# Performance work log

Measured on AMD Instinct MI355X. Metric: run time of the kernel, lower is better.

The kernel has to match this reference:

```python
import jax, jax.numpy as jnp
import numpy as np

N_NODES = 50000
N_EDGES = 600000


def gcn_conv(x, src, dst, W, b, num_nodes):
    # x: [N, Cin] -> [N, Cout]; symmetric-normalized GCN with self-loops
    h = x @ W  # [N, Cout]
    loop = jnp.arange(num_nodes, dtype=src.dtype)
    s = jnp.concatenate([src, loop])
    d = jnp.concatenate([dst, loop])
    ones = jnp.ones(s.shape[0], dtype=h.dtype)
    deg = jax.ops.segment_sum(ones, d, num_segments=num_nodes)  # in-degree incl self-loop
    dinv = jnp.where(deg > 0, jax.lax.rsqrt(deg), 0.0)
    norm = dinv[s] * dinv[d]  # [E+N]
    msg = h[s] * norm[:, None]  # gather + scale
    out = jax.ops.segment_sum(msg, d, num_segments=num_nodes)  # scatter-add
    return out + b


def setup_inputs() -> dict:
    key = jax.random.key(0)
    k1, k2, k3, k4 = jax.random.split(key, 4)
    x = jax.random.normal(k1, (N_NODES, 128), dtype=jnp.float32)
    edge_index = jax.random.randint(k2, (2, N_EDGES), 0, N_NODES, dtype=jnp.int64)
    W1 = jax.random.normal(k3, (128, 128), dtype=jnp.float32) * (1.0 / np.sqrt(128))
    b1 = jnp.zeros((128,), dtype=jnp.float32)
    W2 = jax.random.normal(k4, (128, 64), dtype=jnp.float32) * (1.0 / np.sqrt(128))
    b2 = jnp.zeros((64,), dtype=jnp.float32)
    return {"x": x, "edge_index": edge_index, "W1": W1, "b1": b1, "W2": W2, "b2": b2}


def reference(x, edge_index, W1, b1, W2, b2):
    src, dst = edge_index[0], edge_index[1]
    h = gcn_conv(x, src, dst, W1, b1, N_NODES)
    h = jax.nn.relu(h)
    out = gcn_conv(h, src, dst, W2, b2, N_NODES)
    return out
```

## Files before the change

kernel.cpp:

```cpp
#include <hip/hip_runtime.h>
#include <cstddef>
#include <cstdint>

#define N_NODES 50000
#define N_EDGES 600000
#define M_TILES 3125
#define GEMM_BLKS 782
#define NBUCK 196
#define BUCK_CAP 4096
#define ROUTE_EDGES 2048
#define ROUTE_BLKS 293

typedef short bf16x8 __attribute__((ext_vector_type(8)));
typedef float f32x4 __attribute__((ext_vector_type(4)));


__device__ __forceinline__ unsigned short f32_to_bf16(float x) {
  unsigned u = __float_as_uint(x);
  u += 0x7FFFu + ((u >> 16) & 1u);
  return (unsigned short)(u >> 16);
}
__device__ __forceinline__ float bf16_to_f32(unsigned short h) {
  return __uint_as_float((unsigned)h << 16);
}
__device__ __forceinline__ float bf16_lo(unsigned g) {
  return __uint_as_float(g << 16);
}
__device__ __forceinline__ float bf16_hi(unsigned g) {
  return __uint_as_float(g & 0xFFFF0000u);
}

__device__ __forceinline__ void split8(const float* __restrict__ p, bf16x8& hi,
                                       bf16x8& lo) {
  const float4 v0 = *(const float4*)p;
  const float4 v1 = *(const float4*)(p + 4);
  float v[8] = {v0.x, v0.y, v0.z, v0.w, v1.x, v1.y, v1.z, v1.w};
#pragma unroll
  for (int i = 0; i < 8; i++) {
    const unsigned short h = f32_to_bf16(v[i]);
    hi[i] = (short)h;
    lo[i] = (short)f32_to_bf16(v[i] - bf16_to_f32(h));
  }
}

template <int COUT>
__device__ __forceinline__ void gemm_body(const int wtile, const int lane,
                                          const float* __restrict__ X,
                                          const unsigned short* __restrict__ Wph,
                                          const unsigned short* __restrict__ Wpl,
                                          unsigned short* __restrict__ Hs) {
  constexpr int CT = COUT / 16;
  const int m = lane & 15;
  const int q = lane >> 4;

  f32x4 acc[CT];
#pragma unroll
  for (int ct = 0; ct < CT; ct++) acc[ct] = {0.f, 0.f, 0.f, 0.f};

  const float* xp = X + (size_t)(wtile * 16 + m) * 128 + q * 8;

#pragma unroll
  for (int ks = 0; ks < 4; ks++) {
    bf16x8 ah, al;
    split8(xp + ks * 32, ah, al);
#pragma unroll
    for (int ct = 0; ct < CT; ct++) {
      const size_t bo = ((size_t)(ct * 4 + ks) * 64 + lane) * 8;
      const bf16x8 bh = *(const bf16x8*)(Wph + bo);
      const bf16x8 bl = *(const bf16x8*)(Wpl + bo);
      acc[ct] = __builtin_amdgcn_mfma_f32_16x16x32_bf16(ah, bh, acc[ct], 0, 0, 0);
      acc[ct] = __builtin_amdgcn_mfma_f32_16x16x32_bf16(al, bh, acc[ct], 0, 0, 0);
      acc[ct] = __builtin_amdgcn_mfma_f32_16x16x32_bf16(ah, bl, acc[ct], 0, 0, 0);
    }
  }
#pragma unroll
  for (int ct = 0; ct < CT; ct++) {
#pragma unroll
    for (int r = 0; r < 4; r++) {
      const int orow = wtile * 16 + q * 4 + r;
      Hs[(size_t)orow * COUT + ct * 16 + m] = f32_to_bf16(acc[ct][r]);
    }
  }
}

__global__ __launch_bounds__(256) void k_prep_route(
    const float* __restrict__ W1, const float* __restrict__ W2,
    unsigned short* __restrict__ w1h, unsigned short* __restrict__ w1l,
    unsigned short* __restrict__ w2h, unsigned short* __restrict__ w2l,
    const int* __restrict__ src, const int* __restrict__ dst,
    int* __restrict__ cursor, unsigned* __restrict__ routed) {
  __shared__ int hist[NBUCK];
  __shared__ int lcur[NBUCK];
  const int tid = threadIdx.x;
  if (blockIdx.x < 96) {
    const int i = blockIdx.x * 256 + tid;
    const float* W;
    unsigned short *wh, *wl;
    int o, cout;
    if (i < 16384) {
      W = W1; wh = w1h; wl = w1l; o = i; cout = 128;
    } else {
      W = W2; wh = w2h; wl = w2l; o = i - 16384; cout = 64;
    }
    const int j = o & 7;
    const int lane = (o >> 3) & 63;
    const int t = o >> 9;
    const int ks = t & 3;
    const int ct = t >> 2;
    const int k = ks * 32 + (lane >> 4) * 8 + j;
    const int n = ct * 16 + (lane & 15);
    const float v = W[k * cout + n];
    const unsigned short h = f32_to_bf16(v);
    wh[o] = h;
    wl[o] = f32_to_bf16(v - bf16_to_f32(h));
  } else {
    const int rb = blockIdx.x - 96;
    for (int t = tid; t < NBUCK; t += 256) hist[t] = 0;
    __syncthreads();
    unsigned packed[8];
    bool cvalid[2];
    const int base = rb * ROUTE_EDGES;
#pragma unroll
    for (int c = 0; c < 2; c++) {
      const int i4 = base + c * 1024 + tid * 4;
      cvalid[c] = (i4 < N_EDGES);
      if (cvalid[c]) {
        const int4 d4 = *(const int4*)(dst + i4);
        const int4 s4 = *(const int4*)(src + i4);
        packed[c * 4 + 0] = ((unsigned)d4.x << 16) | (unsigned)s4.x;
        packed[c * 4 + 1] = ((unsigned)d4.y << 16) | (unsigned)s4.y;
        packed[c * 4 + 2] = ((unsigned)d4.z << 16) | (unsigned)s4.z;
        packed[c * 4 + 3] = ((unsigned)d4.w << 16) | (unsigned)s4.w;
#pragma unroll
        for (int j = 0; j < 4; j++)
          atomicAdd(&hist[packed[c * 4 + j] >> 24], 1);
      }
    }
    __syncthreads();
    for (int t = tid; t < NBUCK; t += 256)
      lcur[t] = t * BUCK_CAP + atomicAdd(&cursor[t], hist[t]);
    __syncthreads();
#pragma unroll
    for (int c = 0; c < 2; c++) {
      if (cvalid[c]) {
#pragma unroll
        for (int j = 0; j < 4; j++) {
          const unsigned pk = packed[c * 4 + j];
          const int slot = atomicAdd(&lcur[pk >> 24], 1);
          routed[slot] = pk;
        }
      }
    }
  }
}

__global__ __launch_bounds__(256) void k_bsort_gemm128(
    const unsigned* __restrict__ routed, const int* __restrict__ cursor,
    int* __restrict__ counts, int* __restrict__ start,
    int* __restrict__ sorted_src, const float* __restrict__ X,
    const unsigned short* __restrict__ Wph,
    const unsigned short* __restrict__ Wpl, unsigned short* __restrict__ Hs) {
  __shared__ unsigned ebuf[BUCK_CAP];
  __shared__ int h2[256];
  __shared__ int c2[256];
  const int tid = threadIdx.x;
  if (blockIdx.x < NBUCK) {
    const int b = blockIdx.x;
    const int n = cursor[b];
    for (int i = tid; i < n; i += 256) ebuf[i] = routed[b * BUCK_CAP + i];
    h2[tid] = 0;
    __syncthreads();
    for (int i = tid; i < n; i += 256)
      atomicAdd(&h2[(ebuf[i] >> 16) & 255], 1);
    __syncthreads();
    const int own = h2[tid];
    for (int s = 1; s < 256; s <<= 1) {
      const int t = (tid >= s) ? h2[tid - s] : 0;
      __syncthreads();
      h2[tid] += t;
      __syncthreads();
    }
    const int pfx = h2[tid] - own;
    c2[tid] = pfx;
    const int d = b * 256 + tid;
    if (d < N_NODES) {
      counts[d] = own;
      start[d] = b * BUCK_CAP + pfx;
    }
    __syncthreads();
    for (int i = tid; i < n; i += 256) {
      const unsigned pk = ebuf[i];
      const int r = atomicAdd(&c2[(pk >> 16) & 255], 1);
      sorted_src[b * BUCK_CAP + r] = (int)(pk & 0xFFFFu);
    }
  } else {
    const int wtile = (blockIdx.x - NBUCK) * 4 + (tid >> 6);
    if (wtile < M_TILES) gemm_body<128>(wtile, tid & 63, X, Wph, Wpl, Hs);
  }
}

__global__ __launch_bounds__(256) void k_agg128_gemm64(
    const unsigned* __restrict__ Hb, const int* __restrict__ counts,
    const int* __restrict__ start, const int* __restrict__ sorted_src,
    const float* __restrict__ bias, const unsigned short* __restrict__ Wph,
    const unsigned short* __restrict__ Wpl, unsigned short* __restrict__ Hs) {
  __shared__ float a1s[16][132];
  const int lane = threadIdx.x & 63;
  const int wave = threadIdx.x >> 6;
  const int h = lane >> 5;
  const int c = lane & 31;
  const uint2* __restrict__ Hb2 = (const uint2*)Hb;
  const float4 bb = ((const float4*)bias)[c];
  const int vbase = blockIdx.x * 16 + wave * 4;

#pragma unroll
  for (int p = 0; p < 2; p++) {
    const int v = vbase + 2 * p + h;
    const int deg = counts[v];
    const int e0 = start[v];
    const float dv = rsqrtf((float)deg + 1.0f);
    const uint2 gs = Hb2[(size_t)v * 32 + c];
    int si = 0;
    float wi = 0.f;
    if (c < deg) {
      si = sorted_src[e0 + c];
      wi = rsqrtf((float)counts[si] + 1.0f) * dv;
    }
    const int dA = __shfl(deg, 0);
    const int dB = __shfl(deg, 32);
    const int mm = max(dA, dB);
    const int m = min(mm, 32);
    const float dv2 = dv * dv;
    float a0 = bf16_lo(gs.x) * dv2;
    float a1 = bf16_hi(gs.x) * dv2;
    float a2 = bf16_lo(gs.y) * dv2;
    float a3 = bf16_hi(gs.y) * dv2;

    for (int j = 0; j < m; j += 8) {
      int s[8];
      float w[8];
      uint2 g[8];
#pragma unroll
      for (int t = 0; t < 8; t++) {
        s[t] = __shfl(si, (lane & 32) | (j + t));
        w[t] = __shfl(wi, (lane & 32) | (j + t));
      }
#pragma unroll
      for (int t = 0; t < 8; t++) g[t] = Hb2[(size_t)s[t] * 32 + c];
#pragma unroll
      for (int t = 0; t < 8; t++) {
        a0 += bf16_lo(g[t].x) * w[t];
        a1 += bf16_hi(g[t].x) * w[t];
        a2 += bf16_lo(g[t].y) * w[t];
        a3 += bf16_hi(g[t].y) * w[t];
      }
    }
    for (int base = 32; base < mm; base += 32) {
      int sit = 0;
      float wit = 0.f;
      if (base + c < deg) {
        sit = sorted_src[e0 + base + c];
        wit = rsqrtf((float)counts[sit] + 1.0f) * dv;
      }
      const int lim = min(32, mm - base);
      for (int k = 0; k < lim; k++) {
        const int s = __shfl(sit, (lane & 32) | k);
        const float w = __shfl(wit, (lane & 32) | k);
        const uint2 g = Hb2[(size_t)s * 32 + c];
        a0 += bf16_lo(g.x) * w;
        a1 += bf16_hi(g.x) * w;
        a2 += bf16_lo(g.y) * w;
        a3 += bf16_hi(g.y) * w;
      }
    }
    float4 r;
    r.x = fmaxf(a0 + bb.x, 0.f);
    r.y = fmaxf(a1 + bb.y, 0.f);
    r.z = fmaxf(a2 + bb.z, 0.f);
    r.w = fmaxf(a3 + bb.w, 0.f);
    *(float4*)&a1s[wave * 4 + 2 * p + h][c * 4] = r;
  }
  __syncthreads();

  const int ct = wave;
  const int m = lane & 15;
  const int q = lane >> 4;
  f32x4 acc = {0.f, 0.f, 0.f, 0.f};
#pragma unroll
  for (int ks = 0; ks < 4; ks++) {
    bf16x8 ah, al;
    split8(&a1s[m][ks * 32 + q * 8], ah, al);
    const size_t bo = ((size_t)(ct * 4 + ks) * 64 + lane) * 8;
    const bf16x8 bh = *(const bf16x8*)(Wph + bo);
    const bf16x8 bl = *(const bf16x8*)(Wpl + bo);
    acc = __builtin_amdgcn_mfma_f32_16x16x32_bf16(ah, bh, acc, 0, 0, 0);
    acc = __builtin_amdgcn_mfma_f32_16x16x32_bf16(al, bh, acc, 0, 0, 0);
    acc = __builtin_amdgcn_mfma_f32_16x16x32_bf16(ah, bl, acc, 0, 0, 0);
  }
#pragma unroll
  for (int r = 0; r < 4; r++) {
    const int orow = blockIdx.x * 16 + q * 4 + r;
    Hs[(size_t)orow * 64 + ct * 16 + m] = f32_to_bf16(acc[r]);
  }
}

__global__ __launch_bounds__(256) void k_agg64(
    const unsigned* __restrict__ Hb, const int* __restrict__ counts,
    const int* __restrict__ start, const int* __restrict__ sorted_src,
    const float* __restrict__ bias, float* __restrict__ out) {
  const int lane = threadIdx.x & 63;
  const int wave = threadIdx.x >> 6;
  const int qq = lane >> 4;
  const int c = lane & 15;
  const uint2* __restrict__ Hb2 = (const uint2*)Hb;
  const float4 bb = ((const float4*)bias)[c];

  const int v = blockIdx.x * 16 + wave * 4 + qq;
  const int deg = counts[v];
  const int e0 = start[v];
  const float dv = rsqrtf((float)deg + 1.0f);
  const uint2 gs = Hb2[(size_t)v * 16 + c];
  int si0 = 0, si1 = 0;
  float wi0 = 0.f, wi1 = 0.f;
  if (c < deg) {
    si0 = sorted_src[e0 + c];
    wi0 = rsqrtf((float)counts[si0] + 1.0f) * dv;
  }
  if (c + 16 < deg) {
    si1 = sorted_src[e0 + c + 16];
    wi1 = rsqrtf((float)counts[si1] + 1.0f) * dv;
  }
  const int d0 = __shfl(deg, 0);
  const int d1 = __shfl(deg, 16);
  const int d2 = __shfl(deg, 32);
  const int d3 = __shfl(deg, 48);
  const int mm = max(max(d0, d1), max(d2, d3));
  const int m = min(mm, 32);
  const float dv2 = dv * dv;
  float a0 = bf16_lo(gs.x) * dv2;
  float a1 = bf16_hi(gs.x) * dv2;
  float a2 = bf16_lo(gs.y) * dv2;
  float a3 = bf16_hi(gs.y) * dv2;

#pragma unroll
  for (int jb = 0; jb < 4; jb++) {
    if (jb * 8 < m) {
      int s[8];
      float w[8];
      uint2 g[8];
#pragma unroll
      for (int t = 0; t < 8; t++) {
        const int e = jb * 8 + t;
        const int srcl = (lane & 48) | (e & 15);
        s[t] = __shfl((jb < 2) ? si0 : si1, srcl);
        w[t] = __shfl((jb < 2) ? wi0 : wi1, srcl);
      }
#pragma unroll
      for (int t = 0; t < 8; t++) g[t] = Hb2[(size_t)s[t] * 16 + c];
#pragma unroll
      for (int t = 0; t < 8; t++) {
        a0 += bf16_lo(g[t].x) * w[t];
        a1 += bf16_hi(g[t].x) * w[t];
        a2 += bf16_lo(g[t].y) * w[t];
        a3 += bf16_hi(g[t].y) * w[t];
      }
    }
  }
  for (int base = 32; base < mm; base += 16) {
    int sit = 0;
    float wit = 0.f;
    if (base + c < deg) {
      sit = sorted_src[e0 + base + c];
      wit = rsqrtf((float)counts[sit] + 1.0f) * dv;
    }
    const int lim = min(16, mm - base);
    for (int k = 0; k < lim; k++) {
      const int s = __shfl(sit, (lane & 48) | k);
      const float w = __shfl(wit, (lane & 48) | k);
      const uint2 g = Hb2[(size_t)s * 16 + c];
      a0 += bf16_lo(g.x) * w;
      a1 += bf16_hi(g.x) * w;
      a2 += bf16_lo(g.y) * w;
      a3 += bf16_hi(g.y) * w;
    }
  }
  float4 r;
  r.x = a0 + bb.x;
  r.y = a1 + bb.y;
  r.z = a2 + bb.z;
  r.w = a3 + bb.w;
  ((float4*)out)[(size_t)v * 16 + c] = r;
}


extern "C" void kernel_launch(void* const* d_in, const int* in_sizes, int n_in,
                              void* d_out, int out_size, void* d_ws, size_t ws_size,
                              hipStream_t stream) {
  const float* x = (const float*)d_in[0];
  const int* ei = (const int*)d_in[1];
  const float* W1 = (const float*)d_in[2];
  const float* b1 = (const float*)d_in[3];
  const float* W2 = (const float*)d_in[4];
  const float* b2 = (const float*)d_in[5];
  const int* src = ei;
  const int* dst = ei + N_EDGES;

  char* p = (char*)d_ws;
  auto alloc = [&](size_t bytes) {
    char* q = p;
    p += (bytes + 255) & ~(size_t)255;
    return q;
  };
  int* cursor = (int*)alloc((size_t)NBUCK * 4);
  unsigned* routed = (unsigned*)alloc((size_t)NBUCK * BUCK_CAP * 4);
  int* sorted_src = (int*)alloc((size_t)NBUCK * BUCK_CAP * 4);
  int* counts = (int*)alloc((size_t)N_NODES * 4);
  int* start = (int*)alloc((size_t)N_NODES * 4);
  unsigned short* w1h = (unsigned short*)alloc(16384 * 2);
  unsigned short* w1l = (unsigned short*)alloc(16384 * 2);
  unsigned short* w2h = (unsigned short*)alloc(8192 * 2);
  unsigned short* w2l = (unsigned short*)alloc(8192 * 2);
  unsigned short* h1b = (unsigned short*)alloc((size_t)N_NODES * 128 * 2);
  unsigned short* h2b = (unsigned short*)alloc((size_t)N_NODES * 64 * 2);

  hipMemsetAsync(cursor, 0, (size_t)NBUCK * 4, stream);
  hipLaunchKernelGGL(k_prep_route, dim3(96 + ROUTE_BLKS), dim3(256), 0, stream,
                     W1, W2, w1h, w1l, w2h, w2l, src, dst, cursor, routed);
  hipLaunchKernelGGL(k_bsort_gemm128, dim3(NBUCK + GEMM_BLKS), dim3(256), 0,
                     stream, routed, cursor, counts, start, sorted_src, x, w1h,
                     w1l, h1b);
  hipLaunchKernelGGL(k_agg128_gemm64, dim3(M_TILES), dim3(256), 0, stream,
                     (const unsigned*)h1b, counts, start, sorted_src, b1, w2h,
                     w2l, h2b);
  hipLaunchKernelGGL(k_agg64, dim3(M_TILES), dim3(256), 0, stream,
                     (const unsigned*)h2b, counts, start, sorted_src, b2,
                     (float*)d_out);
}
```

Before: 152.9 us.

## Fuse all GCN stages into one cooperative persistent kernel with grid syncs

```diff
diff --git a/kernel.cpp b/kernel.cpp
--- a/kernel.cpp
+++ b/kernel.cpp
@@ -1,15 +1,21 @@
 #include <hip/hip_runtime.h>
+#include <hip/hip_cooperative_groups.h>
 #include <cstddef>
 #include <cstdint>
+
+namespace cg = cooperative_groups;
 
 #define N_NODES 50000
 #define N_EDGES 600000
 #define M_TILES 3125
+#define GEMM_UNITS 782
 #define GEMM_BLKS 782
 #define NBUCK 196
 #define BUCK_CAP 4096
 #define ROUTE_EDGES 2048
+#define ROUTE_UNITS 293
 #define ROUTE_BLKS 293
+#define GRID_BLKS 512
 
 typedef short bf16x8 __attribute__((ext_vector_type(8)));
 typedef float f32x4 __attribute__((ext_vector_type(4)));
@@ -82,6 +88,340 @@
     }
   }
 }
+
+__device__ __forceinline__ void wpack_body(const int i,
+                                           const float* __restrict__ W1,
+                                           const float* __restrict__ W2,
+                                           unsigned short* __restrict__ w1h,
+                                           unsigned short* __restrict__ w1l,
+                                           unsigned short* __restrict__ w2h,
+                                           unsigned short* __restrict__ w2l) {
+  const float* W;
+  unsigned short *wh, *wl;
+  int o, cout;
+  if (i < 16384) {
+    W = W1; wh = w1h; wl = w1l; o = i; cout = 128;
+  } else {
+    W = W2; wh = w2h; wl = w2l; o = i - 16384; cout = 64;
+  }
+  const int j = o & 7;
+  const int ln = (o >> 3) & 63;
+  const int t = o >> 9;
+  const int ks = t & 3;
+  const int ct = t >> 2;
+  const int k = ks * 32 + (ln >> 4) * 8 + j;
+  const int n = ct * 16 + (ln & 15);
+  const float v = W[k * cout + n];
+  const unsigned short h = f32_to_bf16(v);
+  wh[o] = h;
+  wl[o] = f32_to_bf16(v - bf16_to_f32(h));
+}
+
+__global__ __launch_bounds__(256, 2) void k_mega(
+    const float* __restrict__ X, const int* __restrict__ src,
+    const int* __restrict__ dst, const float* __restrict__ W1,
+    const float* __restrict__ b1, const float* __restrict__ W2,
+    const float* __restrict__ b2, int* __restrict__ cursor,
+    unsigned* __restrict__ routed, int* __restrict__ sorted_src,
+    int* __restrict__ counts, int* __restrict__ start,
+    unsigned short* __restrict__ w1h, unsigned short* __restrict__ w1l,
+    unsigned short* __restrict__ w2h, unsigned short* __restrict__ w2l,
+    unsigned short* __restrict__ h1b, unsigned short* __restrict__ h2b,
+    float* __restrict__ out) {
+  __shared__ __align__(16) unsigned char smem[BUCK_CAP * 4 + 2048];
+  cg::grid_group grid = cg::this_grid();
+  const int tid = threadIdx.x;
+  const int bid = blockIdx.x;
+  const int lane = tid & 63;
+  const int wave = tid >> 6;
+
+  if (bid < 96) {
+    wpack_body(bid * 256 + tid, W1, W2, w1h, w1l, w2h, w2l);
+  } else if (bid == 96) {
+    if (tid < NBUCK) cursor[tid] = 0;
+  }
+  __threadfence();
+  grid.sync();
+  __threadfence();
+
+  for (int u = bid; u < ROUTE_UNITS + GEMM_UNITS; u += GRID_BLKS) {
+    if (u < ROUTE_UNITS) {
+      int* hist = (int*)smem;
+      int* lcur = hist + NBUCK;
+      for (int t = tid; t < NBUCK; t += 256) hist[t] = 0;
+      __syncthreads();
+      unsigned packed[8];
+      bool cvalid[2];
+      const int base = u * ROUTE_EDGES;
+#pragma unroll
+      for (int c = 0; c < 2; c++) {
+        const int i4 = base + c * 1024 + tid * 4;
+        cvalid[c] = (i4 < N_EDGES);
+        if (cvalid[c]) {
+          const int4 d4 = *(const int4*)(dst + i4);
+          const int4 s4 = *(const int4*)(src + i4);
+          packed[c * 4 + 0] = ((unsigned)d4.x << 16) | (unsigned)s4.x;
+          packed[c * 4 + 1] = ((unsigned)d4.y << 16) | (unsigned)s4.y;
+          packed[c * 4 + 2] = ((unsigned)d4.z << 16) | (unsigned)s4.z;
+          packed[c * 4 + 3] = ((unsigned)d4.w << 16) | (unsigned)s4.w;
+#pragma unroll
+          for (int j = 0; j < 4; j++)
+            atomicAdd(&hist[packed[c * 4 + j] >> 24], 1);
+        }
+      }
+      __syncthreads();
+      for (int t = tid; t < NBUCK; t += 256)
+        lcur[t] = t * BUCK_CAP + atomicAdd(&cursor[t], hist[t]);
+      __syncthreads();
+#pragma unroll
+      for (int c = 0; c < 2; c++) {
+        if (cvalid[c]) {
+#pragma unroll
+          for (int j = 0; j < 4; j++) {
+            const unsigned pk = packed[c * 4 + j];
+            const int slot = atomicAdd(&lcur[pk >> 24], 1);
+            routed[slot] = pk;
+          }
+        }
+      }
+      __syncthreads();
+    } else {
+      const int wtile = (u - ROUTE_UNITS) * 4 + wave;
+      if (wtile < M_TILES) gemm_body<128>(wtile, lane, X, w1h, w1l, h1b);
+    }
+  }
+  __threadfence();
+  grid.sync();
+  __threadfence();
+
+  for (int b = bid; b < NBUCK; b += GRID_BLKS) {
+    unsigned* ebuf = (unsigned*)smem;
+    int* h2 = (int*)(smem + BUCK_CAP * 4);
+    int* c2 = h2 + 256;
+    const int n = cursor[b];
+    for (int i = tid; i < n; i += 256) ebuf[i] = routed[b * BUCK_CAP + i];
+    h2[tid] = 0;
+    __syncthreads();
+    for (int i = tid; i < n; i += 256)
+      atomicAdd(&h2[(ebuf[i] >> 16) & 255], 1);
+    __syncthreads();
+    const int own = h2[tid];
+    for (int s = 1; s < 256; s <<= 1) {
+      const int t = (tid >= s) ? h2[tid - s] : 0;
+      __syncthreads();
+      h2[tid] += t;
+      __syncthreads();
+    }
+    const int pfx = h2[tid] - own;
+    c2[tid] = pfx;
+    const int d = b * 256 + tid;
+    if (d < N_NODES) {
+      counts[d] = own;
+      start[d] = b * BUCK_CAP + pfx;
+    }
+    __syncthreads();
+    for (int i = tid; i < n; i += 256) {
+      const unsigned pk = ebuf[i];
+      const int r = atomicAdd(&c2[(pk >> 16) & 255], 1);
+      sorted_src[b * BUCK_CAP + r] = (int)(pk & 0xFFFFu);
+    }
+    __syncthreads();
+  }
+  __threadfence();
+  grid.sync();
+  __threadfence();
+
+  {
+    float(*a1s)[132] = (float(*)[132])smem;
+    const int h = lane >> 5;
+    const int c = lane & 31;
+    const uint2* __restrict__ Hb2 = (const uint2*)h1b;
+    const float4 bb = ((const float4*)b1)[c];
+
+    for (int u = bid; u < M_TILES; u += GRID_BLKS) {
+      const int vbase = u * 16 + wave * 4;
+#pragma unroll
+      for (int p = 0; p < 2; p++) {
+        const int v = vbase + 2 * p + h;
+        const int deg = counts[v];
+        const int e0 = start[v];
+        const float dv = rsqrtf((float)deg + 1.0f);
+        const uint2 gs = Hb2[(size_t)v * 32 + c];
+        int si = 0;
+        float wi = 0.f;
+        if (c < deg) {
+          si = sorted_src[e0 + c];
+          wi = rsqrtf((float)counts[si] + 1.0f) * dv;
+        }
+        const int dA = __shfl(deg, 0);
+        const int dB = __shfl(deg, 32);
+        const int mm = max(dA, dB);
+        const int m = min(mm, 32);
+        const float dv2 = dv * dv;
+        float a0 = bf16_lo(gs.x) * dv2;
+        float a1 = bf16_hi(gs.x) * dv2;
+        float a2 = bf16_lo(gs.y) * dv2;
+        float a3 = bf16_hi(gs.y) * dv2;
+
+        for (int j = 0; j < m; j += 8) {
+          int s[8];
+          float w[8];
+          uint2 g[8];
+#pragma unroll
+          for (int t = 0; t < 8; t++) {
+            s[t] = __shfl(si, (lane & 32) | (j + t));
+            w[t] = __shfl(wi, (lane & 32) | (j + t));
+          }
+#pragma unroll
+          for (int t = 0; t < 8; t++) g[t] = Hb2[(size_t)s[t] * 32 + c];
+#pragma unroll
+          for (int t = 0; t < 8; t++) {
+            a0 += bf16_lo(g[t].x) * w[t];
+            a1 += bf16_hi(g[t].x) * w[t];
+            a2 += bf16_lo(g[t].y) * w[t];
+            a3 += bf16_hi(g[t].y) * w[t];
+          }
+        }
+        for (int base = 32; base < mm; base += 32) {
+          int sit = 0;
+          float wit = 0.f;
+          if (base + c < deg) {
+            sit = sorted_src[e0 + base + c];
+            wit = rsqrtf((float)counts[sit] + 1.0f) * dv;
+          }
+          const int lim = min(32, mm - base);
+          for (int k = 0; k < lim; k++) {
+            const int s = __shfl(sit, (lane & 32) | k);
+            const float w = __shfl(wit, (lane & 32) | k);
+            const uint2 g = Hb2[(size_t)s * 32 + c];
+            a0 += bf16_lo(g.x) * w;
+            a1 += bf16_hi(g.x) * w;
+            a2 += bf16_lo(g.y) * w;
+            a3 += bf16_hi(g.y) * w;
+          }
+        }
+        float4 r;
+        r.x = fmaxf(a0 + bb.x, 0.f);
+        r.y = fmaxf(a1 + bb.y, 0.f);
+        r.z = fmaxf(a2 + bb.z, 0.f);
+        r.w = fmaxf(a3 + bb.w, 0.f);
+        *(float4*)&a1s[wave * 4 + 2 * p + h][c * 4] = r;
+      }
+      __syncthreads();
+
+      const int ct = wave;
+      const int m2 = lane & 15;
+      const int q = lane >> 4;
+      f32x4 acc = {0.f, 0.f, 0.f, 0.f};
+#pragma unroll
+      for (int ks = 0; ks < 4; ks++) {
+        bf16x8 ah, al;
+        split8(&a1s[m2][ks * 32 + q * 8], ah, al);
+        const size_t bo = ((size_t)(ct * 4 + ks) * 64 + lane) * 8;
+        const bf16x8 bh = *(const bf16x8*)(w2h + bo);
+        const bf16x8 bl = *(const bf16x8*)(w2l + bo);
+        acc = __builtin_amdgcn_mfma_f32_16x16x32_bf16(ah, bh, acc, 0, 0, 0);
+        acc = __builtin_amdgcn_mfma_f32_16x16x32_bf16(al, bh, acc, 0, 0, 0);
+        acc = __builtin_amdgcn_mfma_f32_16x16x32_bf16(ah, bl, acc, 0, 0, 0);
+      }
+#pragma unroll
+      for (int r = 0; r < 4; r++) {
+        const int orow = u * 16 + q * 4 + r;
+        h2b[(size_t)orow * 64 + ct * 16 + m2] = f32_to_bf16(acc[r]);
+      }
+      __syncthreads();
+    }
+  }
+  __threadfence();
+  grid.sync();
+  __threadfence();
+
+  {
+    const int qq = lane >> 4;
+    const int c = lane & 15;
+    const uint2* __restrict__ Hb2 = (const uint2*)h2b;
+    const float4 bb = ((const float4*)b2)[c];
+
+    for (int u = bid; u < M_TILES; u += GRID_BLKS) {
+      const int v = u * 16 + wave * 4 + qq;
+      const int deg = counts[v];
+      const int e0 = start[v];
+      const float dv = rsqrtf((float)deg + 1.0f);
+      const uint2 gs = Hb2[(size_t)v * 16 + c];
+      int si0 = 0, si1 = 0;
+      float wi0 = 0.f, wi1 = 0.f;
+      if (c < deg) {
+        si0 = sorted_src[e0 + c];
+        wi0 = rsqrtf((float)counts[si0] + 1.0f) * dv;
+      }
+      if (c + 16 < deg) {
+        si1 = sorted_src[e0 + c + 16];
+        wi1 = rsqrtf((float)counts[si1] + 1.0f) * dv;
+      }
+      const int d0 = __shfl(deg, 0);
+      const int d1 = __shfl(deg, 16);
+      const int d2 = __shfl(deg, 32);
+      const int d3 = __shfl(deg, 48);
+      const int mm = max(max(d0, d1), max(d2, d3));
+      const int m = min(mm, 32);
+      const float dv2 = dv * dv;
+      float a0 = bf16_lo(gs.x) * dv2;
+      float a1 = bf16_hi(gs.x) * dv2;
+      float a2 = bf16_lo(gs.y) * dv2;
+      float a3 = bf16_hi(gs.y) * dv2;
+
+#pragma unroll
+      for (int jb = 0; jb < 4; jb++) {
+        if (jb * 8 < m) {
+          int s[8];
+          float w[8];
+          uint2 g[8];
+#pragma unroll
+          for (int t = 0; t < 8; t++) {
+            const int e = jb * 8 + t;
+            const int srcl = (lane & 48) | (e & 15);
+            s[t] = __shfl((jb < 2) ? si0 : si1, srcl);
+            w[t] = __shfl((jb < 2) ? wi0 : wi1, srcl);
+          }
+#pragma unroll
+          for (int t = 0; t < 8; t++) g[t] = Hb2[(size_t)s[t] * 16 + c];
+#pragma unroll
+          for (int t = 0; t < 8; t++) {
+            a0 += bf16_lo(g[t].x) * w[t];
+            a1 += bf16_hi(g[t].x) * w[t];
+            a2 += bf16_lo(g[t].y) * w[t];
+            a3 += bf16_hi(g[t].y) * w[t];
+          }
+        }
+      }
+      for (int base = 32; base < mm; base += 16) {
+        int sit = 0;
+        float wit = 0.f;
+        if (base + c < deg) {
+          sit = sorted_src[e0 + base + c];
+          wit = rsqrtf((float)counts[sit] + 1.0f) * dv;
+        }
+        const int lim = min(16, mm - base);
+        for (int k = 0; k < lim; k++) {
+          const int s = __shfl(sit, (lane & 48) | k);
+          const float w = __shfl(wit, (lane & 48) | k);
+          const uint2 g = Hb2[(size_t)s * 16 + c];
+          a0 += bf16_lo(g.x) * w;
+          a1 += bf16_hi(g.x) * w;
+          a2 += bf16_lo(g.y) * w;
+          a3 += bf16_hi(g.y) * w;
+        }
+      }
+      float4 r;
+      r.x = a0 + bb.x;
+      r.y = a1 + bb.y;
+      r.z = a2 + bb.z;
+      r.w = a3 + bb.w;
+      ((float4*)out)[(size_t)v * 16 + c] = r;
+    }
+  }
+}
+
 
 __global__ __launch_bounds__(256) void k_prep_route(
     const float* __restrict__ W1, const float* __restrict__ W2,
@@ -93,26 +433,7 @@
   __shared__ int lcur[NBUCK];
   const int tid = threadIdx.x;
   if (blockIdx.x < 96) {
-    const int i = blockIdx.x * 256 + tid;
-    const float* W;
-    unsigned short *wh, *wl;
-    int o, cout;
-    if (i < 16384) {
-      W = W1; wh = w1h; wl = w1l; o = i; cout = 128;
-    } else {
-      W = W2; wh = w2h; wl = w2l; o = i - 16384; cout = 64;
-    }
-    const int j = o & 7;
-    const int lane = (o >> 3) & 63;
-    const int t = o >> 9;
-    const int ks = t & 3;
-    const int ct = t >> 2;
-    const int k = ks * 32 + (lane >> 4) * 8 + j;
-    const int n = ct * 16 + (lane & 15);
-    const float v = W[k * cout + n];
-    const unsigned short h = f32_to_bf16(v);
-    wh[o] = h;
-    wl[o] = f32_to_bf16(v - bf16_to_f32(h));
+    wpack_body(blockIdx.x * 256 + tid, W1, W2, w1h, w1l, w2h, w2l);
   } else {
     const int rb = blockIdx.x - 96;
     for (int t = tid; t < NBUCK; t += 256) hist[t] = 0;
@@ -404,6 +725,7 @@
   const float* b2 = (const float*)d_in[5];
   const int* src = ei;
   const int* dst = ei + N_EDGES;
+  float* outp = (float*)d_out;
 
   char* p = (char*)d_ws;
   auto alloc = [&](size_t bytes) {
@@ -423,16 +745,42 @@
   unsigned short* h1b = (unsigned short*)alloc((size_t)N_NODES * 128 * 2);
   unsigned short* h2b = (unsigned short*)alloc((size_t)N_NODES * 64 * 2);
 
-  hipMemsetAsync(cursor, 0, (size_t)NBUCK * 4, stream);
-  hipLaunchKernelGGL(k_prep_route, dim3(96 + ROUTE_BLKS), dim3(256), 0, stream,
-                     W1, W2, w1h, w1l, w2h, w2l, src, dst, cursor, routed);
-  hipLaunchKernelGGL(k_bsort_gemm128, dim3(NBUCK + GEMM_BLKS), dim3(256), 0,
-                     stream, routed, cursor, counts, start, sorted_src, x, w1h,
-                     w1l, h1b);
-  hipLaunchKernelGGL(k_agg128_gemm64, dim3(M_TILES), dim3(256), 0, stream,
-                     (const unsigned*)h1b, counts, start, sorted_src, b1, w2h,
-                     w2l, h2b);
-  hipLaunchKernelGGL(k_agg64, dim3(M_TILES), dim3(256), 0, stream,
-                     (const unsigned*)h2b, counts, start, sorted_src, b2,
-                     (float*)d_out);
-}
+  static int coop_ok = -1;
+  if (coop_ok < 0) {
+    int coop_attr = 0;
+    if (hipDeviceGetAttribute(&coop_attr, hipDeviceAttributeCooperativeLaunch,
+                              0) != hipSuccess)
+      coop_attr = 0;
+    int max_blk = 0;
+    if (hipOccupancyMaxActiveBlocksPerMultiprocessor(&max_blk, k_mega, 256,
+                                                     0) != hipSuccess)
+      max_blk = 0;
+    coop_ok = (coop_attr != 0 && max_blk >= 2) ? 1 : 0;
+  }
+
+  bool launched = false;
+  if (coop_ok == 1) {
+    void* args[] = {&x,      &src,    &dst,        &W1,     &b1,    &W2,  &b2,
+                    &cursor, &routed, &sorted_src, &counts, &start, &w1h, &w1l,
+                    &w2h,    &w2l,    &h1b,        &h2b,    &outp};
+    const hipError_t err = hipLaunchCooperativeKernel(
+        (const void*)k_mega, dim3(GRID_BLKS), dim3(256), args, 0, stream);
+    launched = (err == hipSuccess);
+  }
+
+  if (!launched) {
+    hipMemsetAsync(cursor, 0, (size_t)NBUCK * 4, stream);
+    hipLaunchKernelGGL(k_prep_route, dim3(96 + ROUTE_BLKS), dim3(256), 0,
+                       stream, W1, W2, w1h, w1l, w2h, w2l, src, dst, cursor,
+                       routed);
+    hipLaunchKernelGGL(k_bsort_gemm128, dim3(NBUCK + GEMM_BLKS), dim3(256), 0,
+                       stream, routed, cursor, counts, start, sorted_src, x,
+                       w1h, w1l, h1b);
+    hipLaunchKernelGGL(k_agg128_gemm64, dim3(M_TILES), dim3(256), 0, stream,
+                       (const unsigned*)h1b, counts, start, sorted_src, b1,
+                       w2h, w2l, h2b);
+    hipLaunchKernelGGL(k_agg64, dim3(M_TILES), dim3(256), 0, stream,
+                       (const unsigned*)h2b, counts, start, sorted_src, b2,
+                       (float*)d_out);
+  }
+}
```

Result: no change. 150.0 us (-1.9%).

## Precompute per-edge source normalization as fp16 packed into sorted_src

Applied to the files above, without the earlier changes.

```diff
diff --git a/kernel.cpp b/kernel.cpp
--- a/kernel.cpp
+++ b/kernel.cpp
@@ -1,4 +1,5 @@
 #include <hip/hip_runtime.h>
+#include <hip/hip_fp16.h>
 #include <cstddef>
 #include <cstdint>
 
@@ -28,6 +29,9 @@
 }
 __device__ __forceinline__ float bf16_hi(unsigned g) {
   return __uint_as_float(g & 0xFFFF0000u);
+}
+__device__ __forceinline__ float pk_w(unsigned pk) {
+  return __half2float(__ushort_as_half((unsigned short)(pk >> 16)));
 }
 
 __device__ __forceinline__ void split8(const float* __restrict__ p, bf16x8& hi,
@@ -83,36 +87,46 @@
   }
 }
 
+__device__ __forceinline__ void wpack_body(const int i,
+                                           const float* __restrict__ W1,
+                                           const float* __restrict__ W2,
+                                           unsigned short* __restrict__ w1h,
+                                           unsigned short* __restrict__ w1l,
+                                           unsigned short* __restrict__ w2h,
+                                           unsigned short* __restrict__ w2l) {
+  const float* W;
+  unsigned short *wh, *wl;
+  int o, cout;
+  if (i < 16384) {
+    W = W1; wh = w1h; wl = w1l; o = i; cout = 128;
+  } else {
+    W = W2; wh = w2h; wl = w2l; o = i - 16384; cout = 64;
+  }
+  const int j = o & 7;
+  const int ln = (o >> 3) & 63;
+  const int t = o >> 9;
+  const int ks = t & 3;
+  const int ct = t >> 2;
+  const int k = ks * 32 + (ln >> 4) * 8 + j;
+  const int n = ct * 16 + (ln & 15);
+  const float v = W[k * cout + n];
+  const unsigned short h = f32_to_bf16(v);
+  wh[o] = h;
+  wl[o] = f32_to_bf16(v - bf16_to_f32(h));
+}
+
 __global__ __launch_bounds__(256) void k_prep_route(
     const float* __restrict__ W1, const float* __restrict__ W2,
     unsigned short* __restrict__ w1h, unsigned short* __restrict__ w1l,
     unsigned short* __restrict__ w2h, unsigned short* __restrict__ w2l,
     const int* __restrict__ src, const int* __restrict__ dst,
-    int* __restrict__ cursor, unsigned* __restrict__ routed) {
+    int* __restrict__ cursor, int* __restrict__ counts,
+    unsigned* __restrict__ routed) {
   __shared__ int hist[NBUCK];
   __shared__ int lcur[NBUCK];
   const int tid = threadIdx.x;
   if (blockIdx.x < 96) {
-    const int i = blockIdx.x * 256 + tid;
-    const float* W;
-    unsigned short *wh, *wl;
-    int o, cout;
-    if (i < 16384) {
-      W = W1; wh = w1h; wl = w1l; o = i; cout = 128;
-    } else {
-      W = W2; wh = w2h; wl = w2l; o = i - 16384; cout = 64;
-    }
-    const int j = o & 7;
-    const int lane = (o >> 3) & 63;
-    const int t = o >> 9;
-    const int ks = t & 3;
-    const int ct = t >> 2;
-    const int k = ks * 32 + (lane >> 4) * 8 + j;
-    const int n = ct * 16 + (lane & 15);
-    const float v = W[k * cout + n];
-    const unsigned short h = f32_to_bf16(v);
-    wh[o] = h;
-    wl[o] = f32_to_bf16(v - bf16_to_f32(h));
+    wpack_body(blockIdx.x * 256 + tid, W1, W2, w1h, w1l, w2h, w2l);
   } else {
     const int rb = blockIdx.x - 96;
     for (int t = tid; t < NBUCK; t += 256) hist[t] = 0;
@@ -132,8 +146,11 @@
         packed[c * 4 + 2] = ((unsigned)d4.z << 16) | (unsigned)s4.z;
         packed[c * 4 + 3] = ((unsigned)d4.w << 16) | (unsigned)s4.w;
 #pragma unroll
-        for (int j = 0; j < 4; j++)
-          atomicAdd(&hist[packed[c * 4 + j] >> 24], 1);
+        for (int j = 0; j < 4; j++) {
+          const unsigned pk = packed[c * 4 + j];
+          atomicAdd(&hist[pk >> 24], 1);
+          atomicAdd(&counts[pk >> 16], 1);
+        }
       }
     }
     __syncthreads();
@@ -156,7 +173,7 @@
 
 __global__ __launch_bounds__(256) void k_bsort_gemm128(
     const unsigned* __restrict__ routed, const int* __restrict__ cursor,
-    int* __restrict__ counts, int* __restrict__ start,
+    const int* __restrict__ counts, int* __restrict__ start,
     int* __restrict__ sorted_src, const float* __restrict__ X,
     const unsigned short* __restrict__ Wph,
     const unsigned short* __restrict__ Wpl, unsigned short* __restrict__ Hs) {
@@ -183,15 +200,15 @@
     const int pfx = h2[tid] - own;
     c2[tid] = pfx;
     const int d = b * 256 + tid;
-    if (d < N_NODES) {
-      counts[d] = own;
-      start[d] = b * BUCK_CAP + pfx;
-    }
+    if (d < N_NODES) start[d] = b * BUCK_CAP + pfx;
     __syncthreads();
     for (int i = tid; i < n; i += 256) {
       const unsigned pk = ebuf[i];
       const int r = atomicAdd(&c2[(pk >> 16) & 255], 1);
-      sorted_src[b * BUCK_CAP + r] = (int)(pk & 0xFFFFu);
+      const unsigned si = pk & 0xFFFFu;
+      const float rs = rsqrtf((float)counts[si] + 1.0f);
+      const unsigned hb = (unsigned)__half_as_ushort(__float2half(rs));
+      sorted_src[b * BUCK_CAP + r] = (int)(si | (hb << 16));
     }
   } else {
     const int wtile = (blockIdx.x - NBUCK) * 4 + (tid >> 6);
@@ -213,19 +230,24 @@
   const float4 bb = ((const float4*)bias)[c];
   const int vbase = blockIdx.x * 16 + wave * 4;
 
+  const int v0 = vbase + h, v1 = vbase + 2 + h;
+  const int deg0 = counts[v0], deg1 = counts[v1];
+  const int e00 = start[v0], e01 = start[v1];
+  const float dv0 = rsqrtf((float)deg0 + 1.f);
+  const float dv1 = rsqrtf((float)deg1 + 1.f);
+  const uint2 gs0 = Hb2[(size_t)v0 * 32 + c];
+  const uint2 gs1 = Hb2[(size_t)v1 * 32 + c];
+  const int pk0 = (c < deg0) ? sorted_src[e00 + c] : 0;
+  const int pk1 = (c < deg1) ? sorted_src[e01 + c] : 0;
+
 #pragma unroll
   for (int p = 0; p < 2; p++) {
-    const int v = vbase + 2 * p + h;
-    const int deg = counts[v];
-    const int e0 = start[v];
-    const float dv = rsqrtf((float)deg + 1.0f);
-    const uint2 gs = Hb2[(size_t)v * 32 + c];
-    int si = 0;
-    float wi = 0.f;
-    if (c < deg) {
-      si = sorted_src[e0 + c];
-      wi = rsqrtf((float)counts[si] + 1.0f) * dv;
-    }
+    const int deg = p ? deg1 : deg0;
+    const int e0 = p ? e01 : e00;
+    const float dv = p ? dv1 : dv0;
+    const uint2 gs = p ? gs1 : gs0;
+    const int pk = p ? pk1 : pk0;
+
     const int dA = __shfl(deg, 0);
     const int dB = __shfl(deg, 32);
     const int mm = max(dA, dB);
@@ -237,16 +259,17 @@
     float a3 = bf16_hi(gs.y) * dv2;
 
     for (int j = 0; j < m; j += 8) {
-      int s[8];
+      unsigned pkt[8];
       float w[8];
       uint2 g[8];
 #pragma unroll
-      for (int t = 0; t < 8; t++) {
-        s[t] = __shfl(si, (lane & 32) | (j + t));
-        w[t] = __shfl(wi, (lane & 32) | (j + t));
-      }
-#pragma unroll
-      for (int t = 0; t < 8; t++) g[t] = Hb2[(size_t)s[t] * 32 + c];
+      for (int t = 0; t < 8; t++)
+        pkt[t] = (unsigned)__shfl(pk, (lane & 32) | (j + t));
+#pragma unroll
+      for (int t = 0; t < 8; t++)
+        g[t] = Hb2[(size_t)(pkt[t] & 0xFFFFu) * 32 + c];
+#pragma unroll
+      for (int t = 0; t < 8; t++) w[t] = pk_w(pkt[t]) * dv;
 #pragma unroll
       for (int t = 0; t < 8; t++) {
         a0 += bf16_lo(g[t].x) * w[t];
@@ -256,17 +279,13 @@
       }
     }
     for (int base = 32; base < mm; base += 32) {
-      int sit = 0;
-      float wit = 0.f;
-      if (base + c < deg) {
-        sit = sorted_src[e0 + base + c];
-        wit = rsqrtf((float)counts[sit] + 1.0f) * dv;
-      }
+      int pk2 = 0;
+      if (base + c < deg) pk2 = sorted_src[e0 + base + c];
       const int lim = min(32, mm - base);
       for (int k = 0; k < lim; k++) {
-        const int s = __shfl(sit, (lane & 32) | k);
-        const float w = __shfl(wit, (lane & 32) | k);
-        const uint2 g = Hb2[(size_t)s * 32 + c];
+        const unsigned pt = (unsigned)__shfl(pk2, (lane & 32) | k);
+        const uint2 g = Hb2[(size_t)(pt & 0xFFFFu) * 32 + c];
+        const float w = pk_w(pt) * dv;
         a0 += bf16_lo(g.x) * w;
         a1 += bf16_hi(g.x) * w;
         a2 += bf16_lo(g.y) * w;
@@ -283,13 +302,13 @@
   __syncthreads();
 
   const int ct = wave;
-  const int m = lane & 15;
+  const int m2 = lane & 15;
   const int q = lane >> 4;
   f32x4 acc = {0.f, 0.f, 0.f, 0.f};
 #pragma unroll
   for (int ks = 0; ks < 4; ks++) {
     bf16x8 ah, al;
-    split8(&a1s[m][ks * 32 + q * 8], ah, al);
+    split8(&a1s[m2][ks * 32 + q * 8], ah, al);
     const size_t bo = ((size_t)(ct * 4 + ks) * 64 + lane) * 8;
     const bf16x8 bh = *(const bf16x8*)(Wph + bo);
     const bf16x8 bl = *(const bf16x8*)(Wpl + bo);
@@ -300,7 +319,7 @@
 #pragma unroll
   for (int r = 0; r < 4; r++) {
     const int orow = blockIdx.x * 16 + q * 4 + r;
-    Hs[(size_t)orow * 64 + ct * 16 + m] = f32_to_bf16(acc[r]);
+    Hs[(size_t)orow * 64 + ct * 16 + m2] = f32_to_bf16(acc[r]);
   }
 }
 
@@ -320,16 +339,9 @@
   const int e0 = start[v];
   const float dv = rsqrtf((float)deg + 1.0f);
   const uint2 gs = Hb2[(size_t)v * 16 + c];
-  int si0 = 0, si1 = 0;
-  float wi0 = 0.f, wi1 = 0.f;
-  if (c < deg) {
-    si0 = sorted_src[e0 + c];
-    wi0 = rsqrtf((float)counts[si0] + 1.0f) * dv;
-  }
-  if (c + 16 < deg) {
-    si1 = sorted_src[e0 + c + 16];
-    wi1 = rsqrtf((float)counts[si1] + 1.0f) * dv;
-  }
+  const int pk0 = (c < deg) ? sorted_src[e0 + c] : 0;
+  const int pk1 = (c + 16 < deg) ? sorted_src[e0 + c + 16] : 0;
+
   const int d0 = __shfl(deg, 0);
   const int d1 = __shfl(deg, 16);
   const int d2 = __shfl(deg, 32);
@@ -345,18 +357,20 @@
 #pragma unroll
   for (int jb = 0; jb < 4; jb++) {
     if (jb * 8 < m) {
-      int s[8];
+      unsigned pkt[8];
       float w[8];
       uint2 g[8];
 #pragma unroll
       for (int t = 0; t < 8; t++) {
         const int e = jb * 8 + t;
         const int srcl = (lane & 48) | (e & 15);
-        s[t] = __shfl((jb < 2) ? si0 : si1, srcl);
-        w[t] = __shfl((jb < 2) ? wi0 : wi1, srcl);
-      }
-#pragma unroll
-      for (int t = 0; t < 8; t++) g[t] = Hb2[(size_t)s[t] * 16 + c];
+        pkt[t] = (unsigned)__shfl((jb < 2) ? pk0 : pk1, srcl);
+      }
+#pragma unroll
+      for (int t = 0; t < 8; t++)
+        g[t] = Hb2[(size_t)(pkt[t] & 0xFFFFu) * 16 + c];
+#pragma unroll
+      for (int t = 0; t < 8; t++) w[t] = pk_w(pkt[t]) * dv;
 #pragma unroll
       for (int t = 0; t < 8; t++) {
         a0 += bf16_lo(g[t].x) * w[t];
@@ -367,17 +381,13 @@
     }
   }
   for (int base = 32; base < mm; base += 16) {
-    int sit = 0;
-    float wit = 0.f;
-    if (base + c < deg) {
-      sit = sorted_src[e0 + base + c];
-      wit = rsqrtf((float)counts[sit] + 1.0f) * dv;
-    }
+    int pk2 = 0;
+    if (base + c < deg) pk2 = sorted_src[e0 + base + c];
     const int lim = min(16, mm - base);
     for (int k = 0; k < lim; k++) {
-      const int s = __shfl(sit, (lane & 48) | k);
-      const float w = __shfl(wit, (lane & 48) | k);
-      const uint2 g = Hb2[(size_t)s * 16 + c];
+      const unsigned pt = (unsigned)__shfl(pk2, (lane & 48) | k);
+      const uint2 g = Hb2[(size_t)(pt & 0xFFFFu) * 16 + c];
+      const float w = pk_w(pt) * dv;
       a0 += bf16_lo(g.x) * w;
       a1 += bf16_hi(g.x) * w;
       a2 += bf16_lo(g.y) * w;
@@ -412,9 +422,9 @@
     return q;
   };
   int* cursor = (int*)alloc((size_t)NBUCK * 4);
+  int* counts = (int*)alloc((size_t)N_NODES * 4);
   unsigned* routed = (unsigned*)alloc((size_t)NBUCK * BUCK_CAP * 4);
   int* sorted_src = (int*)alloc((size_t)NBUCK * BUCK_CAP * 4);
-  int* counts = (int*)alloc((size_t)N_NODES * 4);
   int* start = (int*)alloc((size_t)N_NODES * 4);
   unsigned short* w1h = (unsigned short*)alloc(16384 * 2);
   unsigned short* w1l = (unsigned short*)alloc(16384 * 2);
@@ -423,9 +433,11 @@
   unsigned short* h1b = (unsigned short*)alloc((size_t)N_NODES * 128 * 2);
   unsigned short* h2b = (unsigned short*)alloc((size_t)N_NODES * 64 * 2);
 
-  hipMemsetAsync(cursor, 0, (size_t)NBUCK * 4, stream);
+  const size_t zlen = (size_t)((char*)counts - (char*)cursor) + (size_t)N_NODES * 4;
+  hipMemsetAsync(cursor, 0, zlen, stream);
   hipLaunchKernelGGL(k_prep_route, dim3(96 + ROUTE_BLKS), dim3(256), 0, stream,
-                     W1, W2, w1h, w1l, w2h, w2l, src, dst, cursor, routed);
+                     W1, W2, w1h, w1l, w2h, w2l, src, dst, cursor, counts,
+                     routed);
   hipLaunchKernelGGL(k_bsort_gemm128, dim3(NBUCK + GEMM_BLKS), dim3(256), 0,
                      stream, routed, cursor, counts, start, sorted_src, x, w1h,
                      w1l, h1b);
```

Measured after the change: 170.0 us. 11.2% more time.
